# Performance work log

Measured on AMD Instinct MI355X. Metric: run time of the kernel, lower is better.

Reference implementation:

```python
import jax, jax.numpy as jnp
import numpy as np

B, S, D, H = 2, 2048, 1024, 16
DK = D // H
LARGE = 1e9
LN_EPS = 1e-5


def sinusoidal_embeddings(seq_len, d):
    pos = jnp.arange(seq_len, dtype=jnp.float32)[:, None]          # [S,1]
    i = jnp.arange(d // 2, dtype=jnp.float32)[None, :]             # [1,d/2]
    freq = jnp.exp(-(2.0 * i / d) * jnp.log(10000.0))
    ang = pos * freq                                               # [S,d/2]
    pe = jnp.zeros((seq_len, d), dtype=jnp.float32)
    pe = pe.at[:, 0::2].set(jnp.sin(ang))
    pe = pe.at[:, 1::2].set(jnp.cos(ang))
    return pe


def setup_inputs() -> dict:
    key = jax.random.key(0)
    ks = jax.random.split(key, 6)
    sc = 1.0 / np.sqrt(D)
    return {
        "X": jax.random.normal(ks[0], (B, S, D), jnp.float32),
        "W_q": jax.random.normal(ks[1], (D, D), jnp.float32) * sc,
        "W_k": jax.random.normal(ks[2], (D, D), jnp.float32) * sc,
        "W_v": jax.random.normal(ks[3], (D, D), jnp.float32) * sc,
        "W_o": jax.random.normal(ks[4], (D, D), jnp.float32) * sc,
        "alpha": jnp.ones((1, H, S - 1, 1), jnp.float32),
        "ln_scale": jnp.ones((D,), jnp.float32),
        "ln_bias": jnp.zeros((D,), jnp.float32),
    }


def reference(X, W_q, W_k, W_v, W_o, alpha, ln_scale, ln_bias):
    # projections (torch Linear: x @ W.T), split heads -> [B,H,S,dk]
    def proj(W):
        return jnp.einsum('bsd,ed->bse', X, W).reshape(B, S, H, DK).transpose(0, 2, 1, 3)
    Q, K, V = proj(W_q), proj(W_k), proj(W_v)

    # EMA smear on K along sequence
    a = jax.nn.sigmoid(alpha)                                      # [1,H,S-1,1]
    smeared = K[:, :, 1:, :] * a + K[:, :, :-1, :] * (1.0 - a)
    K = jnp.concatenate([K[:, :, 0:1, :], smeared], axis=2)

    # inline sinusoidal positional embeddings added to K and Q
    pe = sinusoidal_embeddings(S, DK)                              # [S,dk]
    K = K + pe
    Q = Q + pe

    mask = jnp.triu(jnp.ones((S, S), jnp.float32), k=1) * (-LARGE)
    scores = jnp.einsum('bhqd,bhkd->bhqk', Q, K) / jnp.sqrt(jnp.float32(DK)) + mask
    weights = jax.nn.softmax(scores, axis=-1)
    attn = jnp.einsum('bhqk,bhkd->bhqd', weights, V)               # [B,H,S,dk]
    attn = attn.transpose(0, 2, 1, 3).reshape(B, S, D)

    Y = jnp.einsum('bsd,ed->bse', attn, W_o) + X

    # LayerNorm
    mu = jnp.mean(Y, axis=-1, keepdims=True)
    var = jnp.mean(jnp.square(Y - mu), axis=-1, keepdims=True)
    Y = (Y - mu) / jnp.sqrt(var + LN_EPS) * ln_scale + ln_bias
    return Y
```

## Files before the change

kernel.cpp:

```cpp
#include <hip/hip_runtime.h>


#define LB __launch_bounds__(256)

typedef unsigned short u16;
typedef unsigned int u32;
typedef __attribute__((ext_vector_type(2))) unsigned int u32x2;
typedef __attribute__((ext_vector_type(4))) unsigned short us4;
typedef __attribute__((ext_vector_type(8))) unsigned short us8;
typedef __attribute__((ext_vector_type(8))) __bf16 bf8;
typedef __attribute__((ext_vector_type(4))) float f4;
typedef __attribute__((ext_vector_type(4))) short s4;

#define QSCALE 0.18033688011112042f

#if __has_builtin(__builtin_amdgcn_exp2f)
#define EXP2 __builtin_amdgcn_exp2f
#else
#define EXP2 exp2f
#endif

static __device__ __forceinline__ float bf2f(u16 h) {
  union { unsigned int u; float f; } c; c.u = ((unsigned int)h) << 16; return c.f;
}
static __device__ __forceinline__ u16 f2bf(float f) {
  union { float f; unsigned int u; } c; c.f = f;
  unsigned int u = c.u + 0x7FFFu + ((c.u >> 16) & 1u);
  return (u16)(u >> 16);
}
#if __has_builtin(__builtin_amdgcn_cvt_pk_bf16_f32)
typedef __attribute__((ext_vector_type(2))) __bf16 bf2v;
static __device__ __forceinline__ us4 pk_bf16x4(f4 v) {
  bf2v lo = __builtin_amdgcn_cvt_pk_bf16_f32(v[0], v[1]);
  bf2v hi = __builtin_amdgcn_cvt_pk_bf16_f32(v[2], v[3]);
  u32x2 r = {__builtin_bit_cast(u32, lo), __builtin_bit_cast(u32, hi)};
  return __builtin_bit_cast(us4, r);
}
#else
static __device__ __forceinline__ us4 pk_bf16x4(f4 v) {
  return us4{f2bf(v[0]), f2bf(v[1]), f2bf(v[2]), f2bf(v[3])};
}
#endif
static __device__ __forceinline__ float pe_val(int s, int dk) {
  float fr = __expf((float)(dk & ~1) * (-9.210340371976184f / 64.0f));
  float ang = (float)s * fr;
  return (dk & 1) ? __cosf(ang) : __sinf(ang);
}

#if __has_builtin(__builtin_amdgcn_mfma_f32_16x16x16bf16_1k)
static __device__ __forceinline__ f4 mfma16(us4 a, us4 b, f4 c) {
  return __builtin_amdgcn_mfma_f32_16x16x16bf16_1k(
      __builtin_bit_cast(s4, a), __builtin_bit_cast(s4, b), c, 0, 0, 0);
}
#elif __has_builtin(__builtin_amdgcn_mfma_f32_16x16x16_bf16)
typedef __attribute__((ext_vector_type(4))) __bf16 bf4;
static __device__ __forceinline__ f4 mfma16(us4 a, us4 b, f4 c) {
  return __builtin_amdgcn_mfma_f32_16x16x16_bf16(
      __builtin_bit_cast(bf4, a), __builtin_bit_cast(bf4, b), c, 0, 0, 0);
}
#else
static __device__ __forceinline__ f4 mfma16(us4 a, us4 b, f4 c) {
  asm volatile("v_mfma_f32_16x16x16_bf16 %0, %1, %2, %0" : "+v"(c) : "v"(a), "v"(b));
  return c;
}
#endif

#define GLDS(gp, lp) __builtin_amdgcn_global_load_lds( \
    (const __attribute__((address_space(1))) void*)(gp), \
    (__attribute__((address_space(3))) void*)(lp), 16, 0, 0)

__global__ LB void cvt_kernel(const float* __restrict__ X, const float* __restrict__ Wq,
                              const float* __restrict__ Wk, const float* __restrict__ Wv,
                              const float* __restrict__ Wo, u16* __restrict__ Xb,
                              u16* __restrict__ Wcat, u16* __restrict__ Wob) {
  const unsigned t = blockIdx.x * 256 + threadIdx.x;
  const float* src; u16* dst; size_t off;
  if (t < (512u << 10))      { src = X;  dst = Xb;                off = t; }
  else if (t < (640u << 10)) { src = Wq; dst = Wcat;              off = t - (512u << 10); }
  else if (t < (768u << 10)) { src = Wk; dst = Wcat + (1u << 20); off = t - (640u << 10); }
  else if (t < (896u << 10)) { src = Wv; dst = Wcat + (2u << 20); off = t - (768u << 10); }
  else                       { src = Wo; dst = Wob;               off = t - (896u << 10); }
  off *= 8;
  f4 a = *(const f4*)(src + off);
  f4 b = *(const f4*)(src + off + 4);
  us8 o = {f2bf(a[0]), f2bf(a[1]), f2bf(a[2]), f2bf(a[3]),
           f2bf(b[0]), f2bf(b[1]), f2bf(b[2]), f2bf(b[3])};
  *(us8*)(dst + off) = o;
}

static __device__ __forceinline__ void gemm_core(
    const u16* __restrict__ Abase, const u16* __restrict__ Bbase,
    u16* Als, u16* Bls, int m0, int n0, int tid, f4 acc[4][4]) {
  const int w = tid >> 6, lane = tid & 63;
  const int l16 = lane & 15, quad = lane >> 4;
  const int wm = w & 1, wn = w >> 1;
  for (int kk = 0; kk < 1024; kk += 32) {
    __syncthreads();
#pragma unroll
    for (int it = 0; it < 2; it++) {
      int cb = (w * 2 + it) * 64;
      int c = cb + lane;
      int row = c >> 2, kc = c & 3;
      GLDS(Abase + (size_t)(m0 + row) * 1024 + kk + kc * 8, &Als[cb * 8]);
      GLDS(Bbase + (size_t)(n0 + row) * 1024 + kk + kc * 8, &Bls[cb * 8]);
    }
    __syncthreads();
    bf8 af[4], bfr[4];
#pragma unroll
    for (int mt = 0; mt < 4; mt++)
      af[mt] = __builtin_bit_cast(bf8, *(const us8*)(&Als[(wm * 64 + mt * 16 + l16) * 32 + quad * 8]));
#pragma unroll
    for (int nt = 0; nt < 4; nt++)
      bfr[nt] = __builtin_bit_cast(bf8, *(const us8*)(&Bls[(wn * 64 + nt * 16 + l16) * 32 + quad * 8]));
#pragma unroll
    for (int mt = 0; mt < 4; mt++)
#pragma unroll
      for (int nt = 0; nt < 4; nt++)
        acc[mt][nt] = __builtin_amdgcn_mfma_f32_16x16x32_bf16(af[mt], bfr[nt], acc[mt][nt], 0, 0, 0);
  }
}

__global__ LB void gemm_qkv(const u16* __restrict__ Xb, const u16* __restrict__ Wcat,
                            u16* __restrict__ Qb, u16* __restrict__ Kraw,
                            u16* __restrict__ Vp) {
  __shared__ u16 Als[128 * 32];
  __shared__ u16 Bls[128 * 32];
  const int tid = threadIdx.x;
  const int m0 = blockIdx.y * 128, n0 = blockIdx.x * 128;
  f4 acc[4][4];
#pragma unroll
  for (int a = 0; a < 4; a++)
#pragma unroll
    for (int b = 0; b < 4; b++) acc[a][b] = f4{0.f, 0.f, 0.f, 0.f};
  gemm_core(Xb, Wcat, Als, Bls, m0, n0, tid, acc);

  const int w = tid >> 6, lane = tid & 63;
  const int l16 = lane & 15, quad = lane >> 4;
  const int wm = w & 1, wn = w >> 1;
  const int z = blockIdx.x >> 3;
#pragma unroll
  for (int mt = 0; mt < 4; mt++)
#pragma unroll
    for (int nt = 0; nt < 4; nt++)
#pragma unroll
      for (int r = 0; r < 4; r++) {
        int m = m0 + wm * 64 + mt * 16 + quad * 4 + r;
        int nn = (n0 + wn * 64 + nt * 16 + l16) & 1023;
        float v = acc[mt][nt][r];
        int b = m >> 11, s = m & 2047, h = nn >> 6, dk = nn & 63;
        size_t bhoff = (size_t)(b * 16 + h) * (2048 * 64);
        if (z == 0) {
          Qb[bhoff + (size_t)s * 64 + dk] = f2bf((v + pe_val(s, dk)) * QSCALE);
        } else if (z == 1) {
          Kraw[bhoff + (size_t)s * 64 + dk] = f2bf(v);
        } else {
          int kb = s >> 6, sl = s & 63;
          int t = sl >> 4, Qq = (sl >> 2) & 3, jj = sl & 3;
          int dn = dk >> 4, lv = dk & 15;
          Vp[bhoff + (size_t)kb * 4096 + ((t * 4 + dn) * 64 + Qq * 16 + lv) * 4 + jj] = f2bf(v);
        }
      }
}

__global__ LB void ema_pe(const u16* __restrict__ Kraw, const float* __restrict__ alpha,
                          u16* __restrict__ Kp) {
  int idx = blockIdx.x * 256 + threadIdx.x;
  int b8  = idx & 7;
  int s   = (idx >> 3) & 2047;
  int bh  = idx >> 14;
  int dk8 = b8 * 8;
  size_t base = ((size_t)bh * 2048 + s) * 64 + dk8;
  us8 kc = *(const us8*)(Kraw + base);
  float kv[8];
#pragma unroll
  for (int j = 0; j < 8; j++) kv[j] = bf2f(kc[j]);
  if (s > 0) {
    us8 kp = *(const us8*)(Kraw + base - 64);
    float aa = alpha[(bh & 15) * 2047 + s - 1];
    float a = 1.0f / (1.0f + __expf(-aa));
#pragma unroll
    for (int j = 0; j < 8; j++) kv[j] = kv[j] * a + bf2f(kp[j]) * (1.0f - a);
  }
  us8 o;
#pragma unroll
  for (int j = 0; j < 8; j++) o[j] = f2bf(kv[j] + pe_val(s, dk8 + j));
  int kt16 = s >> 4, c = b8 >> 2, quad = b8 & 3, l16s = s & 15;
  size_t off = (size_t)bh * (2048 * 64) + (size_t)kt16 * 1024 + (c * 64 + quad * 16 + l16s) * 8;
  *(us8*)(Kp + off) = o;
}

template<bool MASK>
static __device__ __forceinline__ void attn_step_lds(
    const u16* kbase, const u16* vbase,
    const bf8* qf, f4* acc, float& lsum, int lane, int quad, int qrel0) {
  f4 sc[4];
#pragma unroll
  for (int t = 0; t < 4; t++) sc[t] = f4{0.f, 0.f, 0.f, 0.f};
#pragma unroll
  for (int t = 0; t < 4; t++)
#pragma unroll
    for (int c = 0; c < 2; c++) {
      bf8 kf = __builtin_bit_cast(bf8, *(const us8*)(kbase + (t * 2 + c) * 512 + lane * 8));
      sc[t] = __builtin_amdgcn_mfma_f32_16x16x32_bf16(kf, qf[c], sc[t], 0, 0, 0);
    }
  us4 pf[4];
#pragma unroll
  for (int t = 0; t < 4; t++) {
    f4 pv;
#pragma unroll
    for (int r = 0; r < 4; r++) {
      float s = sc[t][r];
      if (MASK && (t * 16 + quad * 4 + r > qrel0)) s = -1e30f;
      float p = EXP2(s);
      lsum += p;
      pv[r] = p;
    }
    pf[t] = pk_bf16x4(pv);
  }
#pragma unroll
  for (int t = 0; t < 4; t++)
#pragma unroll
    for (int dn = 0; dn < 4; dn++) {
      us4 vf = *(const us4*)(vbase + ((t * 4 + dn) * 64 + lane) * 4);
      acc[dn] = mfma16(vf, pf[t], acc[dn]);
    }
}

__global__ LB void attn_kernel(const u16* __restrict__ Qb, const u16* __restrict__ Kp,
                               const u16* __restrict__ Vp, u16* __restrict__ Ab) {
  __shared__ u16 Kls[2][4096];
  __shared__ u16 Vls[2][4096];
  const int tid = threadIdx.x, w = tid >> 6, lane = tid & 63;
  const int l16 = lane & 15, quad = lane >> 4;
  const int idx = blockIdx.x;
  const int bh = idx & 31;
  const int p  = idx >> 5;
  const size_t bhoff = (size_t)bh * (2048 * 64);
  const u16* Kt = Kp + bhoff;
  const u16* Vt = Vp + bhoff;
  const int b = bh >> 4, h = bh & 15;

  for (int ph = 0; ph < 2; ph++) {
    const int g = ph ? p : 31 - p;
    const int T = g + 1;
    const int qw = g * 64 + w * 16;

    bf8 qf[2];
#pragma unroll
    for (int c = 0; c < 2; c++)
      qf[c] = __builtin_bit_cast(bf8, *(const us8*)(Qb + bhoff + (size_t)(qw + l16) * 64 + c * 32 + quad * 8));

    f4 acc[4];
#pragma unroll
    for (int dn = 0; dn < 4; dn++) acc[dn] = f4{0.f, 0.f, 0.f, 0.f};
    float lsum = 0.f;

    {
      const u16* kg = Kt + w * 1024;
      const u16* vg = Vt + w * 1024;
      GLDS(kg + lane * 8,       &Kls[0][w * 1024]);
      GLDS(kg + 512 + lane * 8, &Kls[0][w * 1024 + 512]);
      GLDS(vg + lane * 8,       &Vls[0][w * 1024]);
      GLDS(vg + 512 + lane * 8, &Vls[0][w * 1024 + 512]);
    }
    asm volatile("s_waitcnt vmcnt(0)" ::: "memory");
    __builtin_amdgcn_s_barrier();

    for (int kb = 0; kb < T; kb++) {
      const int cur = kb & 1;
      if (kb + 1 < T) {
        const u16* kg = Kt + (size_t)(kb + 1) * 4096 + w * 1024;
        const u16* vg = Vt + (size_t)(kb + 1) * 4096 + w * 1024;
        u16* kl = &Kls[cur ^ 1][w * 1024];
        u16* vl = &Vls[cur ^ 1][w * 1024];
        GLDS(kg + lane * 8, kl);
        GLDS(kg + 512 + lane * 8, kl + 512);
        GLDS(vg + lane * 8, vl);
        GLDS(vg + 512 + lane * 8, vl + 512);
      }
      if (kb == T - 1)
        attn_step_lds<true>(&Kls[cur][0], &Vls[cur][0], qf, acc, lsum, lane, quad, w * 16 + l16);
      else
        attn_step_lds<false>(&Kls[cur][0], &Vls[cur][0], qf, acc, lsum, lane, quad, 0);
      asm volatile("s_waitcnt vmcnt(0)" ::: "memory");
      __builtin_amdgcn_s_barrier();
    }

    lsum += __shfl_xor(lsum, 16, 64);
    lsum += __shfl_xor(lsum, 32, 64);
    float rinv = 1.0f / lsum;
    const int q = qw + l16;
    u16* orow = Ab + ((size_t)(b * 2048 + q)) * 1024 + h * 64;
#pragma unroll
    for (int dn = 0; dn < 4; dn++) {
      us4 o = pk_bf16x4(f4{acc[dn][0] * rinv, acc[dn][1] * rinv,
                           acc[dn][2] * rinv, acc[dn][3] * rinv});
      *(us4*)(orow + dn * 16 + quad * 4) = o;
    }
  }
}

__global__ LB void gemm_out(const u16* __restrict__ Ab, const u16* __restrict__ Wob,
                            const float* __restrict__ X, float* __restrict__ Yp) {
  __shared__ u16 Als[128 * 32];
  __shared__ u16 Bls[128 * 32];
  const int tid = threadIdx.x;
  const int m0 = blockIdx.y * 128, n0 = blockIdx.x * 128;
  f4 acc[4][4];
#pragma unroll
  for (int a = 0; a < 4; a++)
#pragma unroll
    for (int b = 0; b < 4; b++) acc[a][b] = f4{0.f, 0.f, 0.f, 0.f};
  gemm_core(Ab, Wob, Als, Bls, m0, n0, tid, acc);

  const int w = tid >> 6, lane = tid & 63;
  const int l16 = lane & 15, quad = lane >> 4;
  const int wm = w & 1, wn = w >> 1;
#pragma unroll
  for (int mt = 0; mt < 4; mt++)
#pragma unroll
    for (int nt = 0; nt < 4; nt++)
#pragma unroll
      for (int r = 0; r < 4; r++) {
        int m = m0 + wm * 64 + mt * 16 + quad * 4 + r;
        int n = n0 + wn * 64 + nt * 16 + l16;
        size_t o = (size_t)m * 1024 + n;
        Yp[o] = acc[mt][nt][r] + X[o];
      }
}

__global__ LB void ln_kernel(const float* __restrict__ Y, const float* __restrict__ g,
                             const float* __restrict__ bta, float* __restrict__ out) {
  __shared__ float ls[4], lsq[4];
  const int row = blockIdx.x, tid = threadIdx.x;
  const int w = tid >> 6, lane = tid & 63;
  f4 v = *(const f4*)(Y + (size_t)row * 1024 + tid * 4);
  float s  = v[0] + v[1] + v[2] + v[3];
  float sq = v[0] * v[0] + v[1] * v[1] + v[2] * v[2] + v[3] * v[3];
#pragma unroll
  for (int d = 1; d < 64; d <<= 1) { s += __shfl_xor(s, d, 64); sq += __shfl_xor(sq, d, 64); }
  if (lane == 0) { ls[w] = s; lsq[w] = sq; }
  __syncthreads();
  s  = ls[0] + ls[1] + ls[2] + ls[3];
  sq = lsq[0] + lsq[1] + lsq[2] + lsq[3];
  float mu  = s * (1.0f / 1024.0f);
  float var = sq * (1.0f / 1024.0f) - mu * mu;
  float rs  = rsqrtf(var + 1e-5f);
  f4 o;
#pragma unroll
  for (int j = 0; j < 4; j++) {
    int col = tid * 4 + j;
    o[j] = (v[j] - mu) * rs * g[col] + bta[col];
  }
  *(f4*)(out + (size_t)row * 1024 + tid * 4) = o;
}

extern "C" void kernel_launch(void* const* d_in, const int* in_sizes, int n_in,
                              void* d_out, int out_size, void* d_ws, size_t ws_size,
                              hipStream_t stream) {
  (void)in_sizes; (void)n_in; (void)out_size; (void)ws_size;
  const float* X  = (const float*)d_in[0];
  const float* Wq = (const float*)d_in[1];
  const float* Wk = (const float*)d_in[2];
  const float* Wv = (const float*)d_in[3];
  const float* Wo = (const float*)d_in[4];
  const float* al = (const float*)d_in[5];
  const float* g  = (const float*)d_in[6];
  const float* bt = (const float*)d_in[7];

  char* ws = (char*)d_ws;
  float* Yp   = (float*)(ws);
  u16*   Xb   = (u16*)(ws + ((size_t)16 << 20));
  u16*   Wcat = (u16*)(ws + ((size_t)24 << 20));
  u16*   Wob  = (u16*)(ws + ((size_t)30 << 20));
  u16*   Qb   = (u16*)(ws + ((size_t)32 << 20));
  u16*   Kraw = (u16*)(ws + ((size_t)40 << 20));
  u16*   Ab   = (u16*)(ws + ((size_t)40 << 20));
  u16*   Kp   = (u16*)(ws + ((size_t)48 << 20));
  u16*   Vp   = (u16*)(ws + ((size_t)56 << 20));

  cvt_kernel<<<dim3(4096), 256, 0, stream>>>(X, Wq, Wk, Wv, Wo, Xb, Wcat, Wob);
  gemm_qkv<<<dim3(24, 32), 256, 0, stream>>>(Xb, Wcat, Qb, Kraw, Vp);
  ema_pe<<<dim3(2048), 256, 0, stream>>>(Kraw, al, Kp);
  attn_kernel<<<dim3(512), 256, 0, stream>>>(Qb, Kp, Vp, Ab);
  gemm_out<<<dim3(8, 32), 256, 0, stream>>>(Ab, Wob, X, Yp);
  ln_kernel<<<dim3(4096), 256, 0, stream>>>(Yp, g, bt, (float*)d_out);
}
```

Baseline: 193.5 us.

## Double-buffer GEMM LDS staging, vectorize V stores, shrink output GEMM tile

Both projection GEMMs now use two LDS buffers, so global-to-LDS loads for the next K-slice are issued while MFMAs run on the current one. This removes one barrier per step and hides load latency. The output GEMM switches to 64x128 tiles, doubling its grid from 256 to 512 blocks to fill more CUs. The V-scatter epilogue in gemm_qkv is packed into 4-element vector stores. In exchange, LDS use per block doubles, which may lower occupancy, and the smaller output tiles reuse each loaded operand less.

Measured after the change: 209.7 us. +8.4%, slower.

```diff
diff --git a/kernel.cpp b/kernel.cpp
--- a/kernel.cpp
+++ b/kernel.cpp
@@ -88,43 +88,91 @@
   *(us8*)(dst + off) = o;
 }
 
+static __device__ __forceinline__ void stage128(
+    const u16* __restrict__ Abase, const u16* __restrict__ Bbase,
+    u16* als, u16* bls, int m0, int n0, int kk, int w, int lane) {
+#pragma unroll
+  for (int it = 0; it < 2; it++) {
+    int c = (w * 2 + it) * 64 + lane;
+    int row = c >> 2, kc = c & 3;
+    GLDS(Abase + (size_t)(m0 + row) * 1024 + kk + kc * 8, als + c * 8);
+    GLDS(Bbase + (size_t)(n0 + row) * 1024 + kk + kc * 8, bls + c * 8);
+  }
+}
+static __device__ __forceinline__ void gemm_step128(
+    const u16* __restrict__ als, const u16* __restrict__ bls,
+    int wm, int wn, int l16, int quad, f4 acc[4][4]) {
+  bf8 af[4], bfr[4];
+#pragma unroll
+  for (int mt = 0; mt < 4; mt++)
+    af[mt] = __builtin_bit_cast(bf8, *(const us8*)(&als[(wm * 64 + mt * 16 + l16) * 32 + quad * 8]));
+#pragma unroll
+  for (int nt = 0; nt < 4; nt++)
+    bfr[nt] = __builtin_bit_cast(bf8, *(const us8*)(&bls[(wn * 64 + nt * 16 + l16) * 32 + quad * 8]));
+#pragma unroll
+  for (int mt = 0; mt < 4; mt++)
+#pragma unroll
+    for (int nt = 0; nt < 4; nt++)
+      acc[mt][nt] = __builtin_amdgcn_mfma_f32_16x16x32_bf16(af[mt], bfr[nt], acc[mt][nt], 0, 0, 0);
+}
 static __device__ __forceinline__ void gemm_core(
     const u16* __restrict__ Abase, const u16* __restrict__ Bbase,
-    u16* Als, u16* Bls, int m0, int n0, int tid, f4 acc[4][4]) {
+    u16* Als0, u16* Als1, u16* Bls0, u16* Bls1,
+    int m0, int n0, int tid, f4 acc[4][4]) {
   const int w = tid >> 6, lane = tid & 63;
   const int l16 = lane & 15, quad = lane >> 4;
   const int wm = w & 1, wn = w >> 1;
-  for (int kk = 0; kk < 1024; kk += 32) {
+  stage128(Abase, Bbase, Als0, Bls0, m0, n0, 0, w, lane);
+  __syncthreads();
+#pragma unroll 1
+  for (int kt = 0; kt < 32; kt += 2) {
+    stage128(Abase, Bbase, Als1, Bls1, m0, n0, (kt + 1) * 32, w, lane);
+    gemm_step128(Als0, Bls0, wm, wn, l16, quad, acc);
     __syncthreads();
-#pragma unroll
-    for (int it = 0; it < 2; it++) {
-      int cb = (w * 2 + it) * 64;
-      int c = cb + lane;
-      int row = c >> 2, kc = c & 3;
-      GLDS(Abase + (size_t)(m0 + row) * 1024 + kk + kc * 8, &Als[cb * 8]);
-      GLDS(Bbase + (size_t)(n0 + row) * 1024 + kk + kc * 8, &Bls[cb * 8]);
-    }
+    if (kt + 2 < 32)
+      stage128(Abase, Bbase, Als0, Bls0, m0, n0, (kt + 2) * 32, w, lane);
+    gemm_step128(Als1, Bls1, wm, wn, l16, quad, acc);
     __syncthreads();
-    bf8 af[4], bfr[4];
-#pragma unroll
-    for (int mt = 0; mt < 4; mt++)
-      af[mt] = __builtin_bit_cast(bf8, *(const us8*)(&Als[(wm * 64 + mt * 16 + l16) * 32 + quad * 8]));
-#pragma unroll
-    for (int nt = 0; nt < 4; nt++)
-      bfr[nt] = __builtin_bit_cast(bf8, *(const us8*)(&Bls[(wn * 64 + nt * 16 + l16) * 32 + quad * 8]));
-#pragma unroll
-    for (int mt = 0; mt < 4; mt++)
-#pragma unroll
-      for (int nt = 0; nt < 4; nt++)
-        acc[mt][nt] = __builtin_amdgcn_mfma_f32_16x16x32_bf16(af[mt], bfr[nt], acc[mt][nt], 0, 0, 0);
-  }
+  }
+}
+
+static __device__ __forceinline__ void stage64(
+    const u16* __restrict__ Abase, const u16* __restrict__ Bbase,
+    u16* als, u16* bls, int m0, int n0, int kk, int tid, int w, int lane) {
+  {
+    int c = tid;
+    int row = c >> 2, kc = c & 3;
+    GLDS(Abase + (size_t)(m0 + row) * 1024 + kk + kc * 8, als + c * 8);
+  }
+#pragma unroll
+  for (int it = 0; it < 2; it++) {
+    int c = (w * 2 + it) * 64 + lane;
+    int row = c >> 2, kc = c & 3;
+    GLDS(Bbase + (size_t)(n0 + row) * 1024 + kk + kc * 8, bls + c * 8);
+  }
+}
+static __device__ __forceinline__ void gemm_step64(
+    const u16* __restrict__ als, const u16* __restrict__ bls,
+    int w, int l16, int quad, f4 acc[4][2]) {
+  bf8 af[4], bfr[2];
+#pragma unroll
+  for (int mt = 0; mt < 4; mt++)
+    af[mt] = __builtin_bit_cast(bf8, *(const us8*)(&als[(mt * 16 + l16) * 32 + quad * 8]));
+#pragma unroll
+  for (int nt = 0; nt < 2; nt++)
+    bfr[nt] = __builtin_bit_cast(bf8, *(const us8*)(&bls[(w * 32 + nt * 16 + l16) * 32 + quad * 8]));
+#pragma unroll
+  for (int mt = 0; mt < 4; mt++)
+#pragma unroll
+    for (int nt = 0; nt < 2; nt++)
+      acc[mt][nt] = __builtin_amdgcn_mfma_f32_16x16x32_bf16(af[mt], bfr[nt], acc[mt][nt], 0, 0, 0);
 }
 
 __global__ LB void gemm_qkv(const u16* __restrict__ Xb, const u16* __restrict__ Wcat,
                             u16* __restrict__ Qb, u16* __restrict__ Kraw,
                             u16* __restrict__ Vp) {
-  __shared__ u16 Als[128 * 32];
-  __shared__ u16 Bls[128 * 32];
+  __shared__ u16 Als[2][128 * 32];
+  __shared__ u16 Bls[2][128 * 32];
   const int tid = threadIdx.x;
   const int m0 = blockIdx.y * 128, n0 = blockIdx.x * 128;
   f4 acc[4][4];
@@ -132,7 +180,7 @@
   for (int a = 0; a < 4; a++)
 #pragma unroll
     for (int b = 0; b < 4; b++) acc[a][b] = f4{0.f, 0.f, 0.f, 0.f};
-  gemm_core(Xb, Wcat, Als, Bls, m0, n0, tid, acc);
+  gemm_core(Xb, Wcat, Als[0], Als[1], Bls[0], Bls[1], m0, n0, tid, acc);
 
   const int w = tid >> 6, lane = tid & 63;
   const int l16 = lane & 15, quad = lane >> 4;
@@ -141,25 +189,31 @@
 #pragma unroll
   for (int mt = 0; mt < 4; mt++)
 #pragma unroll
-    for (int nt = 0; nt < 4; nt++)
-#pragma unroll
-      for (int r = 0; r < 4; r++) {
-        int m = m0 + wm * 64 + mt * 16 + quad * 4 + r;
-        int nn = (n0 + wn * 64 + nt * 16 + l16) & 1023;
-        float v = acc[mt][nt][r];
-        int b = m >> 11, s = m & 2047, h = nn >> 6, dk = nn & 63;
-        size_t bhoff = (size_t)(b * 16 + h) * (2048 * 64);
-        if (z == 0) {
-          Qb[bhoff + (size_t)s * 64 + dk] = f2bf((v + pe_val(s, dk)) * QSCALE);
-        } else if (z == 1) {
-          Kraw[bhoff + (size_t)s * 64 + dk] = f2bf(v);
-        } else {
-          int kb = s >> 6, sl = s & 63;
-          int t = sl >> 4, Qq = (sl >> 2) & 3, jj = sl & 3;
-          int dn = dk >> 4, lv = dk & 15;
-          Vp[bhoff + (size_t)kb * 4096 + ((t * 4 + dn) * 64 + Qq * 16 + lv) * 4 + jj] = f2bf(v);
+    for (int nt = 0; nt < 4; nt++) {
+      int mb = m0 + wm * 64 + mt * 16 + quad * 4;
+      int nn = (n0 + wn * 64 + nt * 16 + l16) & 1023;
+      int b = mb >> 11, h = nn >> 6, dk = nn & 63;
+      size_t bhoff = (size_t)(b * 16 + h) * (2048 * 64);
+      if (z == 2) {
+        int s = mb & 2047;
+        int kb = s >> 6, sl = s & 63;
+        int t = sl >> 4, Qq = (sl >> 2) & 3;
+        int dn = dk >> 4, lv = dk & 15;
+        us4 o = pk_bf16x4(acc[mt][nt]);
+        *(us4*)(Vp + bhoff + (size_t)kb * 4096 + ((t * 4 + dn) * 64 + Qq * 16 + lv) * 4) = o;
+      } else {
+#pragma unroll
+        for (int r = 0; r < 4; r++) {
+          int s = (mb + r) & 2047;
+          float v = acc[mt][nt][r];
+          if (z == 0) {
+            Qb[bhoff + (size_t)s * 64 + dk] = f2bf((v + pe_val(s, dk)) * QSCALE);
+          } else {
+            Kraw[bhoff + (size_t)s * 64 + dk] = f2bf(v);
+          }
         }
       }
+    }
 }
 
 __global__ LB void ema_pe(const u16* __restrict__ Kraw, const float* __restrict__ alpha,
@@ -302,28 +356,39 @@
 
 __global__ LB void gemm_out(const u16* __restrict__ Ab, const u16* __restrict__ Wob,
                             const float* __restrict__ X, float* __restrict__ Yp) {
-  __shared__ u16 Als[128 * 32];
-  __shared__ u16 Bls[128 * 32];
+  __shared__ u16 Als[2][64 * 32];
+  __shared__ u16 Bls[2][128 * 32];
   const int tid = threadIdx.x;
-  const int m0 = blockIdx.y * 128, n0 = blockIdx.x * 128;
-  f4 acc[4][4];
-#pragma unroll
-  for (int a = 0; a < 4; a++)
-#pragma unroll
-    for (int b = 0; b < 4; b++) acc[a][b] = f4{0.f, 0.f, 0.f, 0.f};
-  gemm_core(Ab, Wob, Als, Bls, m0, n0, tid, acc);
-
+  const int m0 = blockIdx.y * 64, n0 = blockIdx.x * 128;
   const int w = tid >> 6, lane = tid & 63;
   const int l16 = lane & 15, quad = lane >> 4;
-  const int wm = w & 1, wn = w >> 1;
-#pragma unroll
-  for (int mt = 0; mt < 4; mt++)
-#pragma unroll
-    for (int nt = 0; nt < 4; nt++)
+  f4 acc[4][2];
+#pragma unroll
+  for (int a = 0; a < 4; a++)
+#pragma unroll
+    for (int b = 0; b < 2; b++) acc[a][b] = f4{0.f, 0.f, 0.f, 0.f};
+
+  stage64(Ab, Wob, Als[0], Bls[0], m0, n0, 0, tid, w, lane);
+  __syncthreads();
+#pragma unroll 1
+  for (int kt = 0; kt < 32; kt += 2) {
+    stage64(Ab, Wob, Als[1], Bls[1], m0, n0, (kt + 1) * 32, tid, w, lane);
+    gemm_step64(Als[0], Bls[0], w, l16, quad, acc);
+    __syncthreads();
+    if (kt + 2 < 32)
+      stage64(Ab, Wob, Als[0], Bls[0], m0, n0, (kt + 2) * 32, tid, w, lane);
+    gemm_step64(Als[1], Bls[1], w, l16, quad, acc);
+    __syncthreads();
+  }
+
+#pragma unroll
+  for (int mt = 0; mt < 4; mt++)
+#pragma unroll
+    for (int nt = 0; nt < 2; nt++)
 #pragma unroll
       for (int r = 0; r < 4; r++) {
-        int m = m0 + wm * 64 + mt * 16 + quad * 4 + r;
-        int n = n0 + wn * 64 + nt * 16 + l16;
+        int m = m0 + mt * 16 + quad * 4 + r;
+        int n = n0 + w * 32 + nt * 16 + l16;
         size_t o = (size_t)m * 1024 + n;
         Yp[o] = acc[mt][nt][r] + X[o];
       }
@@ -383,6 +448,6 @@
   gemm_qkv<<<dim3(24, 32), 256, 0, stream>>>(Xb, Wcat, Qb, Kraw, Vp);
   ema_pe<<<dim3(2048), 256, 0, stream>>>(Kraw, al, Kp);
   attn_kernel<<<dim3(512), 256, 0, stream>>>(Qb, Kp, Vp, Ab);
-  gemm_out<<<dim3(8, 32), 256, 0, stream>>>(Ab, Wob, X, Yp);
+  gemm_out<<<dim3(8, 64), 256, 0, stream>>>(Ab, Wob, X, Yp);
   ln_kernel<<<dim3(4096), 256, 0, stream>>>(Yp, g, bt, (float*)d_out);
 }
```
